# Optimization experiments

Hardware: AMD Instinct MI355X
Metric: run time of the kernel (lower is better)

## Reference

```python
import jax, jax.numpy as jnp
import numpy as np

B, C, CE, DK, DV, H, W = 2, 64, 96, 64, 64, 96, 96
EPS = 1e-6


def setup_inputs() -> dict:
    key = jax.random.key(0)
    ks = jax.random.split(key, 8)
    s = lambda fan_in: 1.0 / np.sqrt(fan_in)
    return {
        "x": jax.random.normal(ks[0], (B, C, H, W), jnp.float32),
        "x_enc": jax.random.normal(ks[1], (B, CE, H, W), jnp.float32),
        "Wq": jax.random.uniform(ks[2], (DK, CE), jnp.float32, -s(CE), s(CE)),
        "bq": jax.random.uniform(ks[3], (DK,), jnp.float32, -s(CE), s(CE)),
        "Wk": jax.random.uniform(ks[4], (DK, CE), jnp.float32, -s(CE), s(CE)),
        "bk": jax.random.uniform(ks[5], (DK,), jnp.float32, -s(CE), s(CE)),
        "Wv": jax.random.uniform(ks[6], (DV, C), jnp.float32, -s(C), s(C)),
        "bv": jax.random.uniform(ks[7], (DV,), jnp.float32, -s(C), s(C)),
    }


def _l2norm(t):
    # F.normalize(dim=1): divide by channel-dim L2 norm, clamped at eps
    n = jnp.maximum(jnp.linalg.norm(t, axis=1, keepdims=True), EPS)
    return t / n


def reference(x, x_enc, Wq, bq, Wk, bk, Wv, bv):
    # 1x1 conv projections == pointwise channel GEMMs
    Q = jnp.einsum('oc,bchw->bohw', Wq, x_enc) + bq[None, :, None, None]
    K = jnp.einsum('oc,bchw->bohw', Wk, x_enc) + bk[None, :, None, None]
    V = jnp.einsum('oc,bchw->bohw', Wv, x) + bv[None, :, None, None]
    vshape = V.shape
    Q = _l2norm(Q.reshape(B, DK, H * W))  # [B, dk, L]
    K = _l2norm(K.reshape(B, DK, H * W))
    V = V.reshape(B, DV, H * W)           # [B, dv, L]
    # cosine-similarity attention over all spatial positions: A is [B, L, L]
    A = jax.nn.softmax(jnp.einsum('bqi,bqj->bij', Q, K), axis=-1)
    R = jnp.einsum('bij,bvj->bvi', A, V)   # [B, dv, L]
    return R.reshape(vshape)
```

## Files before the change

kernel.cpp:

```cpp
#include <hip/hip_runtime.h>

#define L_ 9216

typedef unsigned int uint;
typedef unsigned short ushort;
typedef __attribute__((ext_vector_type(8))) short short8;
typedef __attribute__((ext_vector_type(4))) float f32x4;
typedef __attribute__((ext_vector_type(16))) float f32x16;
typedef __attribute__((ext_vector_type(4))) unsigned uint4v;
typedef __attribute__((ext_vector_type(2))) unsigned uint2v;

#define MFMA32(a, b, c) __builtin_amdgcn_mfma_f32_32x32x16_bf16(a, b, c, 0, 0, 0)

#if __has_builtin(__builtin_amdgcn_exp2f)
#define EXP2(x) __builtin_amdgcn_exp2f(x)
#else
#define EXP2(x) exp2f(x)
#endif

#define GLOAD_LDS16(g, l)                                            \
  __builtin_amdgcn_global_load_lds(                                  \
      (const __attribute__((address_space(1))) unsigned int*)(g),    \
      (__attribute__((address_space(3))) unsigned int*)(l), 16, 0, 0)

union B8 {
  uint4v u;
  short8 s;
};

__device__ __forceinline__ ushort f2bf(float f) {
  uint u = __float_as_uint(f);
  return (ushort)((u + 0x7fffu + ((u >> 16) & 1u)) >> 16);
}

__device__ __forceinline__ f32x16 zero16() {
  f32x16 v;
#pragma unroll
  for (int i = 0; i < 16; i++) v[i] = 0.f;
  return v;
}

template <int CC, int TASK>
__device__ __forceinline__ void projm_body(
    const float* __restrict__ X,
    const float* __restrict__ Wf,
    const float* __restrict__ bias,
    ushort* __restrict__ dst) {
  constexpr int NKT = CC / 16;
  const int bx = blockIdx.x;
  const int b = bx / 288;
  const int p0 = (bx - b * 288) * 32;
  const int lane = threadIdx.x;
  const int ql = lane & 31;
  const int hs = lane >> 5;

  const float* Xb = X + (size_t)b * CC * L_ + p0 + ql;
  float xv[NKT * 8];
#pragma unroll
  for (int kt = 0; kt < NKT; kt++)
#pragma unroll
    for (int i = 0; i < 8; i++)
      xv[kt * 8 + i] = Xb[(size_t)(kt * 16 + hs * 8 + i) * L_];

  B8 bfr[NKT];
#pragma unroll
  for (int kt = 0; kt < NKT; kt++)
#pragma unroll
    for (int j = 0; j < 4; j++) {
      uint lo = f2bf(xv[kt * 8 + 2 * j]);
      uint hi = f2bf(xv[kt * 8 + 2 * j + 1]);
      bfr[kt].u[j] = lo | (hi << 16);
    }

  const float* Wr0 = Wf + (size_t)ql * CC + hs * 8;
  const float* Wr1 = Wf + (size_t)(32 + ql) * CC + hs * 8;

  f32x16 a0 = zero16(), a1 = zero16();
#pragma unroll
  for (int kt = 0; kt < NKT; kt++) {
    float4 wa0 = *(const float4*)(Wr0 + kt * 16);
    float4 wb0 = *(const float4*)(Wr0 + kt * 16 + 4);
    float4 wa1 = *(const float4*)(Wr1 + kt * 16);
    float4 wb1 = *(const float4*)(Wr1 + kt * 16 + 4);
    B8 w0, w1;
    w0.u[0] = (uint)f2bf(wa0.x) | ((uint)f2bf(wa0.y) << 16);
    w0.u[1] = (uint)f2bf(wa0.z) | ((uint)f2bf(wa0.w) << 16);
    w0.u[2] = (uint)f2bf(wb0.x) | ((uint)f2bf(wb0.y) << 16);
    w0.u[3] = (uint)f2bf(wb0.z) | ((uint)f2bf(wb0.w) << 16);
    w1.u[0] = (uint)f2bf(wa1.x) | ((uint)f2bf(wa1.y) << 16);
    w1.u[1] = (uint)f2bf(wa1.z) | ((uint)f2bf(wa1.w) << 16);
    w1.u[2] = (uint)f2bf(wb1.x) | ((uint)f2bf(wb1.y) << 16);
    w1.u[3] = (uint)f2bf(wb1.z) | ((uint)f2bf(wb1.w) << 16);
    a0 = MFMA32(w0.s, bfr[kt].s, a0);
    a1 = MFMA32(w1.s, bfr[kt].s, a1);
  }

#pragma unroll
  for (int g = 0; g < 4; g++) {
    float4 b0 = *(const float4*)(bias + 8 * g + 4 * hs);
    float4 b1 = *(const float4*)(bias + 32 + 8 * g + 4 * hs);
    a0[4 * g + 0] += b0.x; a0[4 * g + 1] += b0.y;
    a0[4 * g + 2] += b0.z; a0[4 * g + 3] += b0.w;
    a1[4 * g + 0] += b1.x; a1[4 * g + 1] += b1.y;
    a1[4 * g + 2] += b1.z; a1[4 * g + 3] += b1.w;
  }

  if (TASK < 2) {
    float ss = 0.f;
#pragma unroll
    for (int r = 0; r < 16; r++) ss += a0[r] * a0[r] + a1[r] * a1[r];
    ss += __shfl_xor(ss, 32);
    float i0 = 1.0f / fmaxf(sqrtf(ss), 1e-6f);
    if (TASK == 0) i0 *= 1.44269504f;
    uint* d = (uint*)(dst + ((size_t)(b * L_ + p0 + ql)) * 64);
#pragma unroll
    for (int g = 0; g < 4; g++) {
      uint2v u0, u1;
      u0[0] = (uint)f2bf(a0[4 * g + 0] * i0) | ((uint)f2bf(a0[4 * g + 1] * i0) << 16);
      u0[1] = (uint)f2bf(a0[4 * g + 2] * i0) | ((uint)f2bf(a0[4 * g + 3] * i0) << 16);
      u1[0] = (uint)f2bf(a1[4 * g + 0] * i0) | ((uint)f2bf(a1[4 * g + 1] * i0) << 16);
      u1[1] = (uint)f2bf(a1[4 * g + 2] * i0) | ((uint)f2bf(a1[4 * g + 3] * i0) << 16);
      *(uint2v*)(d + 4 * g + 2 * hs) = u0;
      *(uint2v*)(d + 16 + 4 * g + 2 * hs) = u1;
    }
  } else {
#pragma unroll
    for (int r = 0; r < 16; r++) {
      int dv0 = (r & 3) + 8 * (r >> 2) + 4 * hs;
      dst[(size_t)(b * 64 + dv0) * L_ + p0 + ql] = f2bf(a0[r]);
      dst[(size_t)(b * 64 + 32 + dv0) * L_ + p0 + ql] = f2bf(a1[r]);
    }
  }
}

__global__ __launch_bounds__(64) void projm_kernel(
    const float* __restrict__ x, const float* __restrict__ x_enc,
    const float* __restrict__ Wq, const float* __restrict__ bq,
    const float* __restrict__ Wk, const float* __restrict__ bk,
    const float* __restrict__ Wv, const float* __restrict__ bv,
    ushort* __restrict__ Qb, ushort* __restrict__ Kb,
    ushort* __restrict__ Vb) {
  const int task = blockIdx.y;
  if (task == 0)
    projm_body<96, 0>(x_enc, Wq, bq, Qb);
  else if (task == 1)
    projm_body<96, 1>(x_enc, Wk, bk, Kb);
  else
    projm_body<64, 2>(x, Wv, bv, Vb);
}

__global__ __launch_bounds__(512, 4) void attn_kernel(
    const ushort* __restrict__ Qb, const ushort* __restrict__ Kb,
    const ushort* __restrict__ Vb, ushort* __restrict__ OP,
    float* __restrict__ LB, int tps) {
  __shared__ __align__(16) ushort KV_l[3][2][4096];

  const int nwg = gridDim.x;
  const int chunk = nwg >> 3;
  const int bid = blockIdx.x;
  const int logical = (bid & 7) * chunk + (bid >> 3);
  const int split = logical / 72;
  const int qidx = logical - split * 72;
  const int b = qidx / 36;
  const int q0 = (qidx - b * 36) * 256;

  const int t = threadIdx.x;
  const int lane = t & 63;
  const int w = t >> 6;
  const int ql = lane & 31;
  const int hs = lane >> 5;

  const ushort* Kg = Kb + (size_t)b * L_ * 64;
  const ushort* Vg = Vb + (size_t)b * 64 * L_;

  const int qrow = q0 + w * 32 + ql;
  const ushort* Qr = Qb + ((size_t)(b * L_ + qrow)) * 64 + hs * 8;
  short8 qf[4];
  qf[0] = *(const short8*)(Qr);
  qf[1] = *(const short8*)(Qr + 16);
  qf[2] = *(const short8*)(Qr + 32);
  qf[3] = *(const short8*)(Qr + 48);

  B8 onesu;
  onesu.u[0] = 0x3F803F80u;
  onesu.u[1] = 0x3F803F80u;
  onesu.u[2] = 0x3F803F80u;
  onesu.u[3] = 0x3F803F80u;

  f32x16 o[2];
  o[0] = zero16();
  o[1] = zero16();
  f32x16 od = zero16();
  f32x16 zv = zero16();

  const int ksw = (ql & 7) << 3;
  const char* lds0 = (const char*)&KV_l[0][0][0];
  int arf[4];
#pragma unroll
  for (int m = 0; m < 4; m++)
    arf[m] = (ql * 64 + ((m * 16 + hs * 8) ^ ksw)) * 2;

  const int rr = t >> 3, pl = t & 7;
  const int psrc = (pl ^ (rr & 7)) << 3;
  const int j0base = split * tps * 64;

#define STAGE(buf, j0)                                                     \
  {                                                                        \
    GLOAD_LDS16(Kg + (size_t)(j0)*64 + rr * 64 + psrc,                     \
                &KV_l[buf][0][w * 512]);                                   \
    GLOAD_LDS16(Vg + (size_t)rr * L_ + (j0) + psrc,                        \
                &KV_l[buf][1][w * 512]);                                   \
  }

#define SMPK1(sa, pf, st)                                                  \
  {                                                                        \
    uint Wp[8];                                                            \
    _Pragma("unroll") for (int c = 0; c < 4; c++) _Pragma("unroll")        \
        for (int rp = 0; rp < 2; rp++) {                                   \
      int i0 = 4 * c + 2 * rp;                                             \
      float p0 = EXP2(sa[i0]);                                             \
      float p1 = EXP2(sa[i0 + 1]);                                         \
      Wp[2 * c + rp] = __builtin_amdgcn_perm(__float_as_uint(p1),          \
                                             __float_as_uint(p0),          \
                                             0x07060302u);                 \
    }                                                                      \
    _Pragma("unroll") for (int u = 0; u < 2; u++) {                        \
      auto ra = __builtin_amdgcn_permlane32_swap(Wp[4 * u + 0],            \
                                                 Wp[4 * u + 2], false,     \
                                                 false);                   \
      auto rb = __builtin_amdgcn_permlane32_swap(Wp[4 * u + 1],            \
                                                 Wp[4 * u + 3], false,     \
                                                 false);                   \
      uint4v fw;                                                           \
      fw[0] = ra[0];                                                       \
      fw[1] = rb[0];                                                       \
      fw[2] = ra[1];                                                       \
      fw[3] = rb[1];                                                       \
      pf[(st)*2 + u].u = fw;                                               \
    }                                                                      \
  }

#define PVH(BUF, sA, sB)                                                   \
  {                                                                        \
    __builtin_amdgcn_s_setprio(1);                                         \
    od = MFMA32(onesu.s, pf[sA].s, od);                                    \
    od = MFMA32(onesu.s, pf[sB].s, od);                                    \
    _Pragma("unroll") for (int dt = 0; dt < 2; dt++) {                     \
      short8 vfa = *(const short8*)(lds0 + arf[sA] + (BUF)*16384 + 8192 +  \
                                    dt * 4096);                            \
      short8 vfb = *(const short8*)(lds0 + arf[sB] + (BUF)*16384 + 8192 +  \
                                    dt * 4096);                            \
      o[dt] = MFMA32(vfa, pf[sA].s, o[dt]);                                \
      o[dt] = MFMA32(vfb, pf[sB].s, o[dt]);                                \
    }                                                                      \
    __builtin_amdgcn_s_setprio(0);                                         \
  }

  STAGE(0, j0base);
  STAGE(1, j0base + 64);

  for (int t3 = 0; t3 < tps; t3 += 3) {
#pragma unroll
    for (int ib = 0; ib < 3; ib++) {
      const int tt = t3 + ib;
      if (tt + 1 < tps) {
        asm volatile("s_waitcnt vmcnt(2)" ::: "memory");
      } else {
        asm volatile("s_waitcnt vmcnt(0)" ::: "memory");
      }
      __builtin_amdgcn_s_barrier();
      __builtin_amdgcn_sched_barrier(0);
      if (tt + 2 < tps) {
        STAGE((ib + 2) % 3, j0base + (tt + 2) * 64);
      }

      f32x16 s0, s1;
      __builtin_amdgcn_s_setprio(1);
      {
        short8 kf0 = *(const short8*)(lds0 + arf[0] + ib * 16384);
        short8 kf1 = *(const short8*)(lds0 + arf[0] + ib * 16384 + 4096);
        s0 = MFMA32(kf0, qf[0], zv);
        s1 = MFMA32(kf1, qf[0], zv);
      }
#pragma unroll
      for (int m = 1; m < 4; m++) {
        short8 kf0 = *(const short8*)(lds0 + arf[m] + ib * 16384);
        short8 kf1 = *(const short8*)(lds0 + arf[m] + ib * 16384 + 4096);
        s0 = MFMA32(kf0, qf[m], s0);
        s1 = MFMA32(kf1, qf[m], s1);
      }
      __builtin_amdgcn_s_setprio(0);

      B8 pf[4];
      SMPK1(s0, pf, 0);
      PVH(ib, 0, 1);
      SMPK1(s1, pf, 1);
      PVH(ib, 2, 3);
    }
  }

  if (hs == 0) LB[(size_t)split * 2 * L_ + (size_t)b * L_ + qrow] = od[0];

  ushort* Ob = OP + (size_t)split * 2 * 64 * L_;
#pragma unroll
  for (int dt = 0; dt < 2; dt++)
#pragma unroll
    for (int r = 0; r < 16; r++) {
      int dv = dt * 32 + (r & 3) + 8 * (r >> 2) + 4 * hs;
      Ob[(size_t)(b * 64 + dv) * L_ + qrow] = f2bf(o[dt][r]);
    }
}

template <int NS>
__global__ __launch_bounds__(256) void combine_kernel(
    const ushort* __restrict__ OP, const float* __restrict__ LB,
    float* __restrict__ out) {
  const size_t e = ((size_t)blockIdx.x * 256 + threadIdx.x) * 8;
  const int bdv = (int)(e / L_);
  const int b = bdv >> 6;
  const int q = (int)(e % L_);
  float os[8], ls[8];
#pragma unroll
  for (int i = 0; i < 8; i++) { os[i] = 0.f; ls[i] = 0.f; }
#pragma unroll
  for (int s = 0; s < NS; s++) {
    uint4v pv = *(const uint4v*)(OP + (size_t)s * 2 * 64 * L_ + e);
    const float* lp = LB + (size_t)s * 2 * L_ + (size_t)b * L_ + q;
    f32x4 l0 = *(const f32x4*)(lp);
    f32x4 l1 = *(const f32x4*)(lp + 4);
#pragma unroll
    for (int i = 0; i < 4; i++) {
      os[2 * i] += __uint_as_float(pv[i] << 16);
      os[2 * i + 1] += __uint_as_float(pv[i] & 0xFFFF0000u);
      ls[i] += l0[i];
      ls[4 + i] += l1[i];
    }
  }
  float r[8];
#pragma unroll
  for (int i = 0; i < 8; i++) r[i] = os[i] / ls[i];
  *(f32x4*)(out + e) = *(const f32x4*)&r[0];
  *(f32x4*)(out + e + 4) = *(const f32x4*)&r[4];
}

extern "C" void kernel_launch(void* const* d_in, const int* in_sizes, int n_in,
                              void* d_out, int out_size, void* d_ws, size_t ws_size,
                              hipStream_t stream) {
  const float* x = (const float*)d_in[0];
  const float* x_enc = (const float*)d_in[1];
  const float* Wq = (const float*)d_in[2];
  const float* bq = (const float*)d_in[3];
  const float* Wk = (const float*)d_in[4];
  const float* bk = (const float*)d_in[5];
  const float* Wv = (const float*)d_in[6];
  const float* bv = (const float*)d_in[7];
  float* out = (float*)d_out;

  ushort* Qb = (ushort*)d_ws;
  ushort* Kb = Qb + (size_t)2 * L_ * 64;
  ushort* Vb = Kb + (size_t)2 * L_ * 64;
  const size_t qkv_bytes = (size_t)3 * 2 * L_ * 64 * 2;

  const int SPLIT = 16;
  ushort* OP = (ushort*)((char*)d_ws + qkv_bytes);
  float* LB = (float*)(OP + (size_t)SPLIT * 2 * 64 * L_);

  projm_kernel<<<dim3(576, 3), 64, 0, stream>>>(x, x_enc, Wq, bq, Wk, bk,
                                                Wv, bv, Qb, Kb, Vb);
  attn_kernel<<<72 * SPLIT, 512, 0, stream>>>(Qb, Kb, Vb, OP, LB, 144 / SPLIT);
  const int cgrid = (2 * 64 * L_ / 8) / 256;
  combine_kernel<16><<<cgrid, 256, 0, stream>>>(OP, LB, out);
}
```

Before: 81.53 us.

## Pre-swizzle K/V into MFMA fragment layout and load directly from global

The projection kernel now writes K and V in a layout that matches the MFMA operand fragments, so each lane reads its short8 operand with one contiguous 16-byte load. The attention kernel drops the LDS triple-buffer staging, the barriers and the swizzled LDS reads, and loads K/V fragments straight from global memory (relying on L2 for reuse across the 8 waves). The launch-bounds occupancy hint is also removed. This cuts the LDS traffic and barrier synchronisation, but the loads are no longer prefetched ahead of use, and each wave now fetches the same K/V tile from cache separately, so global/L2 latency may be exposed.

Measured after the change: 96.99 us. 1.19x slower.

```diff
diff --git a/kernel.cpp b/kernel.cpp
--- a/kernel.cpp
+++ b/kernel.cpp
@@ -17,11 +17,6 @@
 #else
 #define EXP2(x) exp2f(x)
 #endif
-
-#define GLOAD_LDS16(g, l)                                            \
-  __builtin_amdgcn_global_load_lds(                                  \
-      (const __attribute__((address_space(1))) unsigned int*)(g),    \
-      (__attribute__((address_space(3))) unsigned int*)(l), 16, 0, 0)
 
 union B8 {
   uint4v u;
@@ -111,24 +106,56 @@
     for (int r = 0; r < 16; r++) ss += a0[r] * a0[r] + a1[r] * a1[r];
     ss += __shfl_xor(ss, 32);
     float i0 = 1.0f / fmaxf(sqrtf(ss), 1e-6f);
-    if (TASK == 0) i0 *= 1.44269504f;
-    uint* d = (uint*)(dst + ((size_t)(b * L_ + p0 + ql)) * 64);
-#pragma unroll
-    for (int g = 0; g < 4; g++) {
-      uint2v u0, u1;
-      u0[0] = (uint)f2bf(a0[4 * g + 0] * i0) | ((uint)f2bf(a0[4 * g + 1] * i0) << 16);
-      u0[1] = (uint)f2bf(a0[4 * g + 2] * i0) | ((uint)f2bf(a0[4 * g + 3] * i0) << 16);
-      u1[0] = (uint)f2bf(a1[4 * g + 0] * i0) | ((uint)f2bf(a1[4 * g + 1] * i0) << 16);
-      u1[1] = (uint)f2bf(a1[4 * g + 2] * i0) | ((uint)f2bf(a1[4 * g + 3] * i0) << 16);
-      *(uint2v*)(d + 4 * g + 2 * hs) = u0;
-      *(uint2v*)(d + 16 + 4 * g + 2 * hs) = u1;
+    if (TASK == 0) {
+      i0 *= 1.44269504f;
+      uint* d = (uint*)(dst + ((size_t)(b * L_ + p0 + ql)) * 64);
+#pragma unroll
+      for (int g = 0; g < 4; g++) {
+        uint2v u0, u1;
+        u0[0] = (uint)f2bf(a0[4 * g + 0] * i0) | ((uint)f2bf(a0[4 * g + 1] * i0) << 16);
+        u0[1] = (uint)f2bf(a0[4 * g + 2] * i0) | ((uint)f2bf(a0[4 * g + 3] * i0) << 16);
+        u1[0] = (uint)f2bf(a1[4 * g + 0] * i0) | ((uint)f2bf(a1[4 * g + 1] * i0) << 16);
+        u1[1] = (uint)f2bf(a1[4 * g + 2] * i0) | ((uint)f2bf(a1[4 * g + 3] * i0) << 16);
+        *(uint2v*)(d + 4 * g + 2 * hs) = u0;
+        *(uint2v*)(d + 16 + 4 * g + 2 * hs) = u1;
+      }
+    } else {
+      const int j = p0 >> 6;
+      const int st = (p0 >> 5) & 1;
+      ushort* Kfb = dst + (size_t)b * L_ * 64;
+#pragma unroll
+      for (int mt = 0; mt < 2; mt++) {
+#pragma unroll
+        for (int rq = 0; rq < 4; rq++) {
+          const float* x = mt ? (const float*)&a1 : (const float*)&a0;
+          int m = mt * 2 + (rq >> 1);
+          int lp = ql + 32 * (rq & 1);
+          uint2v v;
+          v[0] = (uint)f2bf(x[rq * 4 + 0] * i0) |
+                 ((uint)f2bf(x[rq * 4 + 1] * i0) << 16);
+          v[1] = (uint)f2bf(x[rq * 4 + 2] * i0) |
+                 ((uint)f2bf(x[rq * 4 + 3] * i0) << 16);
+          *(uint2v*)(Kfb + (size_t)(j * 8 + st * 4 + m) * 512 + lp * 8 +
+                     4 * hs) = v;
+        }
+      }
     }
   } else {
-#pragma unroll
-    for (int r = 0; r < 16; r++) {
-      int dv0 = (r & 3) + 8 * (r >> 2) + 4 * hs;
-      dst[(size_t)(b * 64 + dv0) * L_ + p0 + ql] = f2bf(a0[r]);
-      dst[(size_t)(b * 64 + 32 + dv0) * L_ + p0 + ql] = f2bf(a1[r]);
+    const int j = p0 >> 6;
+    const int kvo = (p0 & 63) + ql;
+    const int s = kvo >> 4;
+    const int hkv = (kvo >> 3) & 1;
+    const int i = kvo & 7;
+    ushort* Vfb = dst + (size_t)b * L_ * 64;
+#pragma unroll
+    for (int mt = 0; mt < 2; mt++) {
+      const float* x = mt ? (const float*)&a1 : (const float*)&a0;
+#pragma unroll
+      for (int r = 0; r < 16; r++) {
+        int dvl = (r & 3) + 8 * (r >> 2) + 4 * hs;
+        int lp = dvl + 32 * hkv;
+        Vfb[(size_t)(j * 8 + mt * 4 + s) * 512 + lp * 8 + i] = f2bf(x[r]);
+      }
     }
   }
 }
@@ -138,23 +165,21 @@
     const float* __restrict__ Wq, const float* __restrict__ bq,
     const float* __restrict__ Wk, const float* __restrict__ bk,
     const float* __restrict__ Wv, const float* __restrict__ bv,
-    ushort* __restrict__ Qb, ushort* __restrict__ Kb,
-    ushort* __restrict__ Vb) {
+    ushort* __restrict__ Qb, ushort* __restrict__ Kf,
+    ushort* __restrict__ Vf) {
   const int task = blockIdx.y;
   if (task == 0)
     projm_body<96, 0>(x_enc, Wq, bq, Qb);
   else if (task == 1)
-    projm_body<96, 1>(x_enc, Wk, bk, Kb);
+    projm_body<96, 1>(x_enc, Wk, bk, Kf);
   else
-    projm_body<64, 2>(x, Wv, bv, Vb);
-}
-
-__global__ __launch_bounds__(512, 4) void attn_kernel(
-    const ushort* __restrict__ Qb, const ushort* __restrict__ Kb,
-    const ushort* __restrict__ Vb, ushort* __restrict__ OP,
+    projm_body<64, 2>(x, Wv, bv, Vf);
+}
+
+__global__ __launch_bounds__(512) void attn_kernel(
+    const ushort* __restrict__ Qb, const ushort* __restrict__ Kf,
+    const ushort* __restrict__ Vf, ushort* __restrict__ OP,
     float* __restrict__ LB, int tps) {
-  __shared__ __align__(16) ushort KV_l[3][2][4096];
-
   const int nwg = gridDim.x;
   const int chunk = nwg >> 3;
   const int bid = blockIdx.x;
@@ -170,9 +195,6 @@
   const int ql = lane & 31;
   const int hs = lane >> 5;
 
-  const ushort* Kg = Kb + (size_t)b * L_ * 64;
-  const ushort* Vg = Vb + (size_t)b * 64 * L_;
-
   const int qrow = q0 + w * 32 + ql;
   const ushort* Qr = Qb + ((size_t)(b * L_ + qrow)) * 64 + hs * 8;
   short8 qf[4];
@@ -193,24 +215,10 @@
   f32x16 od = zero16();
   f32x16 zv = zero16();
 
-  const int ksw = (ql & 7) << 3;
-  const char* lds0 = (const char*)&KV_l[0][0][0];
-  int arf[4];
-#pragma unroll
-  for (int m = 0; m < 4; m++)
-    arf[m] = (ql * 64 + ((m * 16 + hs * 8) ^ ksw)) * 2;
-
-  const int rr = t >> 3, pl = t & 7;
-  const int psrc = (pl ^ (rr & 7)) << 3;
-  const int j0base = split * tps * 64;
-
-#define STAGE(buf, j0)                                                     \
-  {                                                                        \
-    GLOAD_LDS16(Kg + (size_t)(j0)*64 + rr * 64 + psrc,                     \
-                &KV_l[buf][0][w * 512]);                                   \
-    GLOAD_LDS16(Vg + (size_t)rr * L_ + (j0) + psrc,                        \
-                &KV_l[buf][1][w * 512]);                                   \
-  }
+  const int le = lane * 8;
+  const ushort* Kb0 = Kf + (size_t)b * L_ * 64 + le;
+  const ushort* Vb0 = Vf + (size_t)b * L_ * 64 + le;
+  const int jb = split * tps;
 
 #define SMPK1(sa, pf, st)                                                  \
   {                                                                        \
@@ -240,63 +248,49 @@
     }                                                                      \
   }
 
-#define PVH(BUF, sA, sB)                                                   \
-  {                                                                        \
-    __builtin_amdgcn_s_setprio(1);                                         \
-    od = MFMA32(onesu.s, pf[sA].s, od);                                    \
-    od = MFMA32(onesu.s, pf[sB].s, od);                                    \
-    _Pragma("unroll") for (int dt = 0; dt < 2; dt++) {                     \
-      short8 vfa = *(const short8*)(lds0 + arf[sA] + (BUF)*16384 + 8192 +  \
-                                    dt * 4096);                            \
-      short8 vfb = *(const short8*)(lds0 + arf[sB] + (BUF)*16384 + 8192 +  \
-                                    dt * 4096);                            \
-      o[dt] = MFMA32(vfa, pf[sA].s, o[dt]);                                \
-      o[dt] = MFMA32(vfb, pf[sB].s, o[dt]);                                \
-    }                                                                      \
-    __builtin_amdgcn_s_setprio(0);                                         \
-  }
-
-  STAGE(0, j0base);
-  STAGE(1, j0base + 64);
-
-  for (int t3 = 0; t3 < tps; t3 += 3) {
-#pragma unroll
-    for (int ib = 0; ib < 3; ib++) {
-      const int tt = t3 + ib;
-      if (tt + 1 < tps) {
-        asm volatile("s_waitcnt vmcnt(2)" ::: "memory");
-      } else {
-        asm volatile("s_waitcnt vmcnt(0)" ::: "memory");
-      }
-      __builtin_amdgcn_s_barrier();
-      __builtin_amdgcn_sched_barrier(0);
-      if (tt + 2 < tps) {
-        STAGE((ib + 2) % 3, j0base + (tt + 2) * 64);
-      }
-
-      f32x16 s0, s1;
-      __builtin_amdgcn_s_setprio(1);
-      {
-        short8 kf0 = *(const short8*)(lds0 + arf[0] + ib * 16384);
-        short8 kf1 = *(const short8*)(lds0 + arf[0] + ib * 16384 + 4096);
-        s0 = MFMA32(kf0, qf[0], zv);
-        s1 = MFMA32(kf1, qf[0], zv);
-      }
-#pragma unroll
-      for (int m = 1; m < 4; m++) {
-        short8 kf0 = *(const short8*)(lds0 + arf[m] + ib * 16384);
-        short8 kf1 = *(const short8*)(lds0 + arf[m] + ib * 16384 + 4096);
-        s0 = MFMA32(kf0, qf[m], s0);
-        s1 = MFMA32(kf1, qf[m], s1);
-      }
-      __builtin_amdgcn_s_setprio(0);
-
-      B8 pf[4];
-      SMPK1(s0, pf, 0);
-      PVH(ib, 0, 1);
-      SMPK1(s1, pf, 1);
-      PVH(ib, 2, 3);
-    }
+  for (int tt = 0; tt < tps; tt++) {
+    const size_t jo = (size_t)((jb + tt) * 8) * 512;
+    const ushort* Kt = Kb0 + jo;
+    const ushort* Vt = Vb0 + jo;
+
+    short8 kf0[4], kf1[4];
+#pragma unroll
+    for (int m = 0; m < 4; m++) {
+      kf0[m] = *(const short8*)(Kt + m * 512);
+      kf1[m] = *(const short8*)(Kt + (4 + m) * 512);
+    }
+
+    f32x16 s0, s1;
+    __builtin_amdgcn_s_setprio(1);
+    s0 = MFMA32(kf0[0], qf[0], zv);
+    s1 = MFMA32(kf1[0], qf[0], zv);
+#pragma unroll
+    for (int m = 1; m < 4; m++) {
+      s0 = MFMA32(kf0[m], qf[m], s0);
+      s1 = MFMA32(kf1[m], qf[m], s1);
+    }
+    __builtin_amdgcn_s_setprio(0);
+
+    short8 vf0[4], vf1[4];
+#pragma unroll
+    for (int s = 0; s < 4; s++) {
+      vf0[s] = *(const short8*)(Vt + s * 512);
+      vf1[s] = *(const short8*)(Vt + (4 + s) * 512);
+    }
+
+    B8 pf[4];
+    SMPK1(s0, pf, 0);
+    SMPK1(s1, pf, 1);
+
+    __builtin_amdgcn_s_setprio(1);
+#pragma unroll
+    for (int s = 0; s < 4; s++) od = MFMA32(onesu.s, pf[s].s, od);
+#pragma unroll
+    for (int s = 0; s < 4; s++) {
+      o[0] = MFMA32(vf0[s], pf[s].s, o[0]);
+      o[1] = MFMA32(vf1[s], pf[s].s, o[1]);
+    }
+    __builtin_amdgcn_s_setprio(0);
   }
 
   if (hs == 0) LB[(size_t)split * 2 * L_ + (size_t)b * L_ + qrow] = od[0];
@@ -357,8 +351,8 @@
   float* out = (float*)d_out;
 
   ushort* Qb = (ushort*)d_ws;
-  ushort* Kb = Qb + (size_t)2 * L_ * 64;
-  ushort* Vb = Kb + (size_t)2 * L_ * 64;
+  ushort* Kf = Qb + (size_t)2 * L_ * 64;
+  ushort* Vf = Kf + (size_t)2 * L_ * 64;
   const size_t qkv_bytes = (size_t)3 * 2 * L_ * 64 * 2;
 
   const int SPLIT = 16;
@@ -366,8 +360,8 @@
   float* LB = (float*)(OP + (size_t)SPLIT * 2 * 64 * L_);
 
   projm_kernel<<<dim3(576, 3), 64, 0, stream>>>(x, x_enc, Wq, bq, Wk, bk,
-                                                Wv, bv, Qb, Kb, Vb);
-  attn_kernel<<<72 * SPLIT, 512, 0, stream>>>(Qb, Kb, Vb, OP, LB, 144 / SPLIT);
+                                                Wv, bv, Qb, Kf, Vf);
+  attn_kernel<<<72 * SPLIT, 512, 0, stream>>>(Qb, Kf, Vf, OP, LB, 144 / SPLIT);
   const int cgrid = (2 * 64 * L_ / 8) / 256;
   combine_kernel<16><<<cgrid, 256, 0, stream>>>(OP, LB, out);
 }
```
